# Performance work log

Hardware: AMD Instinct MI355X
Metric: run time of the kernel (lower is better)

## Reference

```python
import jax, jax.numpy as jnp
import numpy as np

N_NODES = 100000
N_EDGES = 1600000
F_IN = 128
H1 = 128
H2 = 128
N_CLASSES = 40


def setup_inputs() -> dict:
    key = jax.random.key(0)
    ks = jax.random.split(key, 8)
    node_features = jax.random.normal(ks[0], (N_NODES, F_IN), dtype=jnp.float32)
    edge_indices = jax.random.randint(ks[1], (2, N_EDGES), 0, N_NODES, dtype=jnp.int32)
    # Glorot-ish init for weights
    W1 = jax.random.normal(ks[2], (F_IN, H1), dtype=jnp.float32) / np.sqrt(F_IN)
    b1 = jnp.zeros((H1,), dtype=jnp.float32)
    W2 = jax.random.normal(ks[3], (H1, H2), dtype=jnp.float32) / np.sqrt(H1)
    b2 = jnp.zeros((H2,), dtype=jnp.float32)
    Wl = jax.random.normal(ks[4], (H2, N_CLASSES), dtype=jnp.float32) / np.sqrt(H2)
    bl = jnp.zeros((N_CLASSES,), dtype=jnp.float32)
    return {
        "node_features": node_features,
        "edge_indices": edge_indices,
        "W1": W1, "b1": b1,
        "W2": W2, "b2": b2,
        "Wl": Wl, "bl": bl,
    }


def _gcn_norm(edge_indices, n_nodes):
    # PyG GCNConv default: add self-loops, symmetric normalization.
    src = jnp.concatenate([edge_indices[0], jnp.arange(n_nodes, dtype=edge_indices.dtype)])
    dst = jnp.concatenate([edge_indices[1], jnp.arange(n_nodes, dtype=edge_indices.dtype)])
    deg = jax.ops.segment_sum(jnp.ones_like(dst, dtype=jnp.float32), dst,
                              num_segments=n_nodes)  # degree over destinations (col)
    deg_inv_sqrt = jnp.where(deg > 0, jax.lax.rsqrt(deg), 0.0)
    norm = deg_inv_sqrt[src] * deg_inv_sqrt[dst]  # (E + N,)
    return src, dst, norm


def _gcn_conv(x, W, b, src, dst, norm, n_nodes):
    xw = x @ W                                    # (N, F_out) dense GEMM
    msg = xw[src] * norm[:, None]                 # gather + scale: (E+N, F_out)
    out = jax.ops.segment_sum(msg, dst, num_segments=n_nodes)  # scatter-add
    return out + b


def reference(node_features, edge_indices, W1, b1, W2, b2, Wl, bl):
    n = node_features.shape[0]
    src, dst, norm = _gcn_norm(edge_indices, n)
    # dropout is identity in eval mode
    x = jax.nn.relu(_gcn_conv(node_features, W1, b1, src, dst, norm, n))
    x = jax.nn.relu(_gcn_conv(x, W2, b2, src, dst, norm, n))
    return x @ Wl + bl  # (N, num_classes)
```

## Files before the change

### kernel.cpp

```cpp
#include <hip/hip_runtime.h>


typedef unsigned int uint32;
typedef unsigned short u16;

#define FD 128

using short8 = __attribute__((ext_vector_type(8))) short;
using f32x4  = __attribute__((ext_vector_type(4))) float;

union U4S8 { uint4 u; short8 s; };

__device__ __forceinline__ u16 f2bf(float f) {
    uint32 u = __float_as_uint(f);
    uint32 r = ((u >> 16) & 1u) + 0x7FFFu;
    return (u16)((u + r) >> 16);
}
__device__ __forceinline__ float bf2f(u16 s) { return __uint_as_float((uint32)s << 16); }
__device__ __forceinline__ float bfLo(uint32 w) { return __uint_as_float(w << 16); }
__device__ __forceinline__ float bfHi(uint32 w) { return __uint_as_float(w & 0xFFFF0000u); }

__global__ void k_beacon(float* __restrict__ out, long long n, float val) {
    long long i = (long long)blockIdx.x * 256 + threadIdx.x;
    if (i < n) out[i] = val;
}

__global__ __launch_bounds__(256) void k_cnt_mgemm(
    const int* __restrict__ dst, int* __restrict__ cnt, int* __restrict__ rank,
    int ne, int nn,
    const float* __restrict__ A, const float* __restrict__ W,
    uint32* __restrict__ yt, int M,
    int ngemm) {
    __shared__ uint4 Bf[4][8][64];

    int bid = blockIdx.x;
    int g5 = bid / 5;
    bool isg = ((bid % 5) == 0) && (g5 < ngemm);
    int t = threadIdx.x;

    if (!isg) {
        int idx = bid - (g5 + 1 < ngemm ? g5 + 1 : ngemm);
        int e = idx * 256 + t;
        if (e < ne) {
            int d = dst[e];
            int a = ((unsigned)d < (unsigned)nn) ? d : nn;
            rank[e] = atomicAdd(&cnt[a], 1);
        }
        return;
    }

    int idx = g5;
    for (int e = t; e < 4 * 8 * 64; e += 256) {
        int kc = e / (8 * 64);
        int rem = e - kc * (8 * 64);
        int ct = rem >> 6;
        int l  = rem & 63;
        int k0 = kc * 32 + (l >> 4) * 8;
        int c  = ct * 16 + (l & 15);
        u16 us[8];
#pragma unroll
        for (int i = 0; i < 8; i++) us[i] = f2bf(W[(size_t)(k0 + i) * 128 + c]);
        uint4 u;
        u.x = (uint32)us[0] | ((uint32)us[1] << 16);
        u.y = (uint32)us[2] | ((uint32)us[3] << 16);
        u.z = (uint32)us[4] | ((uint32)us[5] << 16);
        u.w = (uint32)us[6] | ((uint32)us[7] << 16);
        Bf[kc][ct][l] = u;
    }
    __syncthreads();

    int lane = t & 63, wv = t >> 6;
    int r0 = idx * 64 + wv * 16;
    if (r0 >= M) return;

    int arow = r0 + (lane & 15);
    if (arow >= M) arow = M - 1;
    U4S8 af[4];
#pragma unroll
    for (int kc = 0; kc < 4; kc++) {
        const float4* s = (const float4*)(A + (size_t)arow * FD + kc * 32 + (lane >> 4) * 8);
        float4 v0 = s[0], v1 = s[1];
        uint4 u;
        u.x = (uint32)f2bf(v0.x) | ((uint32)f2bf(v0.y) << 16);
        u.y = (uint32)f2bf(v0.z) | ((uint32)f2bf(v0.w) << 16);
        u.z = (uint32)f2bf(v1.x) | ((uint32)f2bf(v1.y) << 16);
        u.w = (uint32)f2bf(v1.z) | ((uint32)f2bf(v1.w) << 16);
        af[kc].u = u;
    }

    f32x4 acc[8];
#pragma unroll
    for (int ct = 0; ct < 8; ct++) acc[ct] = f32x4{0.f, 0.f, 0.f, 0.f};
#pragma unroll
    for (int kc = 0; kc < 4; kc++) {
#pragma unroll
        for (int ct = 0; ct < 8; ct++) {
            U4S8 b;
            b.u = Bf[kc][ct][lane];
            acc[ct] = __builtin_amdgcn_mfma_f32_16x16x32_bf16(af[kc].s, b.s, acc[ct], 0, 0, 0);
        }
    }

    int rb = r0 + (lane >> 4) * 4;
#pragma unroll
    for (int r = 0; r < 4; r++) {
        int row = rb + r;
#pragma unroll
        for (int ct = 0; ct < 8; ct++) {
            float v = acc[ct][r];
            float vn = __shfl_xor(v, 1);
            if (!(lane & 1) && row < M) {
                uint32 word = (uint32)f2bf(v) | ((uint32)f2bf(vn) << 16);
                yt[(size_t)row * 128 + (ct * 16 + (lane & 15)) / 2] = word;
            }
        }
    }
}

__global__ void k_scan_a(const int* __restrict__ cnt, int* __restrict__ row_start,
                         int* __restrict__ bsum, float* __restrict__ dis, int nn) {
    __shared__ int tmp[256];
    int t = threadIdx.x;
    int i = blockIdx.x * 256 + t;
    int v = (i < nn) ? cnt[i] : 0;
    if (i < nn) dis[i] = rsqrtf((float)(v + 1));
    tmp[t] = v;
    __syncthreads();
    for (int off = 1; off < 256; off <<= 1) {
        int x = (t >= off) ? tmp[t - off] : 0;
        __syncthreads();
        tmp[t] += x;
        __syncthreads();
    }
    if (i < nn) row_start[i] = tmp[t] - v;
    if (t == 255) bsum[blockIdx.x] = tmp[255];
}

__global__ void k_scan_b(int* bsum, int nb) {
    __shared__ int tmp[512];
    __shared__ int carry;
    int t = threadIdx.x;
    if (t == 0) carry = 0;
    __syncthreads();
    for (int base = 0; base < nb; base += 512) {
        int i = base + t;
        int v = (i < nb) ? bsum[i] : 0;
        tmp[t] = v;
        __syncthreads();
        for (int off = 1; off < 512; off <<= 1) {
            int x = (t >= off) ? tmp[t - off] : 0;
            __syncthreads();
            tmp[t] += x;
            __syncthreads();
        }
        if (i < nb) bsum[i] = tmp[t] - v + carry;
        __syncthreads();
        if (t == 0) carry += tmp[511];
        __syncthreads();
    }
}

__global__ void k_scan_c(int* __restrict__ row_start, const int* __restrict__ bsum,
                         const int* __restrict__ cnt, int nn) {
    int i = blockIdx.x * 256 + threadIdx.x;
    if (i < nn) {
        int r = row_start[i] + bsum[blockIdx.x];
        row_start[i] = r;
        if (i == nn - 1) row_start[nn] = r + cnt[i];
    }
}

__global__ __launch_bounds__(256) void k_fill(const int* __restrict__ src,
                                              const int* __restrict__ dst,
                                              const int* __restrict__ rank,
                                              const int* __restrict__ row_start,
                                              int* __restrict__ col_idx,
                                              int ne, int nn) {
    long long base = ((long long)blockIdx.x * 256 + threadIdx.x) * 4;
    if (base + 4 <= (long long)ne) {
        int4 d4 = *(const int4*)(dst + base);
        int4 s4 = *(const int4*)(src + base);
        int4 r4 = *(const int4*)(rank + base);
        int dd[4] = {d4.x, d4.y, d4.z, d4.w};
        int ss[4] = {s4.x, s4.y, s4.z, s4.w};
        int rr[4] = {r4.x, r4.y, r4.z, r4.w};
        int pp[4];
#pragma unroll
        for (int r = 0; r < 4; r++) {
            bool ok = (unsigned)dd[r] < (unsigned)nn;
            int dv = ok ? dd[r] : 0;
            int p = row_start[dv] + rr[r];
            pp[r] = ok ? p : -1;
        }
#pragma unroll
        for (int r = 0; r < 4; r++)
            if ((unsigned)pp[r] < (unsigned)ne) col_idx[pp[r]] = ss[r];
    } else {
        for (long long e = base; e < (long long)ne; e++) {
            int d = dst[e];
            if ((unsigned)d >= (unsigned)nn) continue;
            int p = row_start[d] + rank[e];
            if ((unsigned)p < (unsigned)ne) col_idx[p] = src[e];
        }
    }
}

template <int NOUT, bool INBF, bool OUTBF>
__global__ __launch_bounds__(256) void k_mgemm(const void* __restrict__ Ap,
                                               const float* __restrict__ W,
                                               void* __restrict__ out,
                                               const float* __restrict__ bias,
                                               int M) {
    constexpr int NT = (NOUT + 15) / 16;
    __shared__ uint4 Bf[4][NT][64];

    int t = threadIdx.x;
    for (int e = t; e < 4 * NT * 64; e += 256) {
        int kc = e / (NT * 64);
        int rem = e - kc * (NT * 64);
        int ct = rem >> 6;
        int l  = rem & 63;
        int k0 = kc * 32 + (l >> 4) * 8;
        int c  = ct * 16 + (l & 15);
        u16 us[8];
#pragma unroll
        for (int i = 0; i < 8; i++)
            us[i] = (c < NOUT) ? f2bf(W[(size_t)(k0 + i) * NOUT + c]) : (u16)0;
        uint4 u;
        u.x = (uint32)us[0] | ((uint32)us[1] << 16);
        u.y = (uint32)us[2] | ((uint32)us[3] << 16);
        u.z = (uint32)us[4] | ((uint32)us[5] << 16);
        u.w = (uint32)us[6] | ((uint32)us[7] << 16);
        Bf[kc][ct][l] = u;
    }
    __syncthreads();

    int lane = t & 63, wv = t >> 6;
    int r0 = blockIdx.x * 64 + wv * 16;
    if (r0 >= M) return;

    int arow = r0 + (lane & 15);
    if (arow >= M) arow = M - 1;
    U4S8 af[4];
    if (INBF) {
        const u16* A = (const u16*)Ap;
#pragma unroll
        for (int kc = 0; kc < 4; kc++)
            af[kc].u = *(const uint4*)(A + (size_t)arow * FD + kc * 32 + (lane >> 4) * 8);
    } else {
        const float* A = (const float*)Ap;
#pragma unroll
        for (int kc = 0; kc < 4; kc++) {
            const float4* s = (const float4*)(A + (size_t)arow * FD + kc * 32 + (lane >> 4) * 8);
            float4 v0 = s[0], v1 = s[1];
            uint4 u;
            u.x = (uint32)f2bf(v0.x) | ((uint32)f2bf(v0.y) << 16);
            u.y = (uint32)f2bf(v0.z) | ((uint32)f2bf(v0.w) << 16);
            u.z = (uint32)f2bf(v1.x) | ((uint32)f2bf(v1.y) << 16);
            u.w = (uint32)f2bf(v1.z) | ((uint32)f2bf(v1.w) << 16);
            af[kc].u = u;
        }
    }

    f32x4 acc[NT];
#pragma unroll
    for (int ct = 0; ct < NT; ct++) acc[ct] = f32x4{0.f, 0.f, 0.f, 0.f};
#pragma unroll
    for (int kc = 0; kc < 4; kc++) {
#pragma unroll
        for (int ct = 0; ct < NT; ct++) {
            U4S8 b;
            b.u = Bf[kc][ct][lane];
            acc[ct] = __builtin_amdgcn_mfma_f32_16x16x32_bf16(af[kc].s, b.s, acc[ct], 0, 0, 0);
        }
    }

    int rb = r0 + (lane >> 4) * 4;
    if (OUTBF) {
        uint32* yt = (uint32*)out;
#pragma unroll
        for (int r = 0; r < 4; r++) {
            int row = rb + r;
#pragma unroll
            for (int ct = 0; ct < NT; ct++) {
                float v = acc[ct][r];
                float vn = __shfl_xor(v, 1);
                if (!(lane & 1) && row < M) {
                    uint32 word = (uint32)f2bf(v) | ((uint32)f2bf(vn) << 16);
                    yt[(size_t)row * 128 + (ct * 16 + (lane & 15)) / 2] = word;
                }
            }
        }
    } else {
        float* fo = (float*)out;
#pragma unroll
        for (int r = 0; r < 4; r++) {
            int row = rb + r;
            if (row >= M) continue;
#pragma unroll
            for (int ct = 0; ct < NT; ct++) {
                int c = ct * 16 + (lane & 15);
                if (c < NOUT) {
                    float v = acc[ct][r];
                    if (bias) v += bias[c];
                    fo[(size_t)row * NOUT + c] = v;
                }
            }
        }
    }
}

__global__ __launch_bounds__(256) void k_agg(const uint32* __restrict__ yt,
                                             const float* __restrict__ dis,
                                             const int* __restrict__ row_start,
                                             const int* __restrict__ col_idx,
                                             const float* __restrict__ bias,
                                             uint32* __restrict__ outp,
                                             int nn, int ne) {
    int lane = threadIdx.x & 63;
    int wid  = threadIdx.x >> 6;
    int g    = lane >> 4;
    int sub  = lane & 15;

    float2 bq[4];
#pragma unroll
    for (int k = 0; k < 4; k++) bq[k] = *(const float2*)(bias + (sub * 4 + k) * 2);

    const int stride = gridDim.x * 16;
    for (int n0 = blockIdx.x * 16 + wid * 4; n0 < nn; n0 += stride) {
        int n = n0 + g;
        bool act = n < nn;
        int nl = act ? n : 0;

        float di = dis[nl];
        int jb = row_start[nl];
        int je = row_start[nl + 1];
        if (!act) { jb = 0; je = 0; }
        if (jb < 0) jb = 0;
        if (je > ne) je = ne;
        int deg = je - jb; if (deg < 0) deg = 0;
        int je1 = je - 1;

        uint4 sv = *(const uint4*)(yt + (size_t)nl * 128 + sub * 4);
        float a0 = bfLo(sv.x) * di, a1 = bfHi(sv.x) * di;
        float a2 = bfLo(sv.y) * di, a3 = bfHi(sv.y) * di;
        float a4 = bfLo(sv.z) * di, a5 = bfHi(sv.z) * di;
        float a6 = bfLo(sv.w) * di, a7 = bfHi(sv.w) * di;

        int m = deg;
        m = max(m, __shfl_xor(m, 16));
        m = max(m, __shfl_xor(m, 32));

        for (int base = 0; base < m; base += 8) {
            int jj = jb + base + (sub & 7);
            int jc = jj < je ? jj : je1;
            if (jc < 0) jc = 0;
            int sl = col_idx[jc];
            float ds = 0.f;
            if ((unsigned)sl < (unsigned)nn) ds = dis[sl];
            else sl = 0;

            int ss[8];
            float ww[8];
#pragma unroll
            for (int r = 0; r < 8; r++) {
                int srcLane = (lane & 48) + r;
                int s = __shfl(sl, srcLane);
                float w = __shfl(ds, srcLane);
                ww[r] = (base + r < deg) ? w : 0.f;
                ss[r] = s;
            }
            uint4 uu[8];
#pragma unroll
            for (int r = 0; r < 8; r++)
                uu[r] = *(const uint4*)(yt + (size_t)ss[r] * 128 + sub * 4);
#pragma unroll
            for (int r = 0; r < 8; r++) {
                float wg = ww[r];
                a0 = fmaf(bfLo(uu[r].x), wg, a0); a1 = fmaf(bfHi(uu[r].x), wg, a1);
                a2 = fmaf(bfLo(uu[r].y), wg, a2); a3 = fmaf(bfHi(uu[r].y), wg, a3);
                a4 = fmaf(bfLo(uu[r].z), wg, a4); a5 = fmaf(bfHi(uu[r].z), wg, a5);
                a6 = fmaf(bfLo(uu[r].w), wg, a6); a7 = fmaf(bfHi(uu[r].w), wg, a7);
            }
        }

        if (act) {
            float r0 = fmaxf(fmaf(a0, di, bq[0].x), 0.f);
            float r1 = fmaxf(fmaf(a1, di, bq[0].y), 0.f);
            float r2 = fmaxf(fmaf(a2, di, bq[1].x), 0.f);
            float r3 = fmaxf(fmaf(a3, di, bq[1].y), 0.f);
            float r4 = fmaxf(fmaf(a4, di, bq[2].x), 0.f);
            float r5 = fmaxf(fmaf(a5, di, bq[2].y), 0.f);
            float r6 = fmaxf(fmaf(a6, di, bq[3].x), 0.f);
            float r7 = fmaxf(fmaf(a7, di, bq[3].y), 0.f);
            uint4 o;
            o.x = (uint32)f2bf(r0) | ((uint32)f2bf(r1) << 16);
            o.y = (uint32)f2bf(r2) | ((uint32)f2bf(r3) << 16);
            o.z = (uint32)f2bf(r4) | ((uint32)f2bf(r5) << 16);
            o.w = (uint32)f2bf(r6) | ((uint32)f2bf(r7) << 16);
            *(uint4*)(outp + (size_t)n * 64 + sub * 4) = o;
        }
    }
}

static inline char* carve(char*& p, size_t bytes) {
    char* r = p;
    p += (bytes + 255) & ~(size_t)255;
    return r;
}

extern "C" void kernel_launch(void* const* d_in, const int* in_sizes, int n_in,
                              void* d_out, int out_size, void* d_ws, size_t ws_size,
                              hipStream_t stream) {
    const long long outn = out_size;
    float* dout = (float*)d_out;
    if (n_in < 8) {
        k_beacon<<<(int)((outn + 255) / 256), 256, 0, stream>>>(dout, outn, 888.f);
        return;
    }
    float* X        = (float*)d_in[0];
    const int* ei   = (const int*)d_in[1];
    const float* W1 = (const float*)d_in[2];
    const float* b1 = (const float*)d_in[3];
    const float* W2 = (const float*)d_in[4];
    const float* b2 = (const float*)d_in[5];
    const float* Wl = (const float*)d_in[6];
    const float* bl = (const float*)d_in[7];

    const int H1 = in_sizes[3];
    const int F  = in_sizes[2] / (H1 > 0 ? H1 : 1);
    const int NC = in_sizes[7];
    const int NN = in_sizes[0] / (F > 0 ? F : 1);
    const int NE = in_sizes[1] / 2;
    if (NN <= 0 || NE <= 0 || F != FD || H1 != FD || NC != 40 ||
        (long long)NN * FD != in_sizes[0] || outn != (long long)NN * NC) {
        k_beacon<<<(int)((outn + 255) / 256), 256, 0, stream>>>(dout, outn, 888.f);
        return;
    }

    const int* src = ei;
    const int* dst = ei + NE;
    const int nb = (NN + 255) / 256;

    char* p = (char*)d_ws;
    int*   cnt       = (int*)  carve(p, ((size_t)NN + 1) * 4);
    float* dis       = (float*)carve(p, (size_t)NN * 4);
    int*   bsum      = (int*)  carve(p, (size_t)nb * 4);
    int*   row_start = (int*)  carve(p, ((size_t)NN + 1) * 4);
    u16*   bufA      = (u16*)  carve(p, (size_t)NN * FD * 2);
    size_t needed = (size_t)(p - (char*)d_ws);
    bool in_out = (size_t)NE * 8 <= (size_t)outn * 4;
    int* col_idx;
    int* rank;
    if (in_out) {
        col_idx = (int*)d_out;
        rank = (int*)((char*)d_out + (size_t)NE * 4);
    } else {
        col_idx = (int*)carve(p, (size_t)NE * 4);
        rank = (int*)carve(p, (size_t)NE * 4);
        needed = (size_t)(p - (char*)d_ws);
    }
    if (needed > ws_size) {
        k_beacon<<<(int)((outn + 255) / 256), 256, 0, stream>>>(dout, outn, 999.f);
        return;
    }

    const int ecb1 = (NE + 255) / 256;
    const int ecb4 = (int)(((long long)NE + 1023) / 1024);
    const int gemm_blocks = (NN + 63) / 64;
    int agg_blocks = (NN + 15) / 16;
    if (agg_blocks > 2048) agg_blocks = 2048;

    hipMemsetAsync(cnt, 0, ((size_t)NN + 1) * 4, stream);
    k_cnt_mgemm<<<ecb1 + gemm_blocks, 256, 0, stream>>>(
        dst, cnt, rank, NE, NN,
        X, W1, (uint32*)X, NN, gemm_blocks);
    k_scan_a<<<nb, 256, 0, stream>>>(cnt, row_start, bsum, dis, NN);
    k_scan_b<<<1, 512, 0, stream>>>(bsum, nb);
    k_scan_c<<<nb, 256, 0, stream>>>(row_start, bsum, cnt, NN);
    k_fill<<<ecb4, 256, 0, stream>>>(src, dst, rank, row_start, col_idx, NE, NN);

    k_agg<<<agg_blocks, 256, 0, stream>>>((const uint32*)X, dis, row_start, col_idx,
                                          b1, (uint32*)bufA, NN, NE);
    k_mgemm<128, true, true><<<gemm_blocks, 256, 0, stream>>>(bufA, W2, X, nullptr, NN);
    k_agg<<<agg_blocks, 256, 0, stream>>>((const uint32*)X, dis, row_start, col_idx,
                                          b2, (uint32*)bufA, NN, NE);
    k_mgemm<40, true, false><<<gemm_blocks, 256, 0, stream>>>(bufA, Wl, dout, bl, NN);
}
```

Before: 362.6 us.

## Fuse neighbor aggregation with following dense GEMM via shared-memory tile

Merges each aggregation kernel with the subsequent MFMA GEMM: a block aggregates 64 node rows into an LDS tile in bf16, then multiplies by the staged weight tile directly. The intermediate bf16 buffer round trip through global memory and two launches are removed. The second layer's source-side normalization is folded into the first fused kernel's output scaling, so the second aggregation runs unweighted. It also moves col_idx into the workspace and writes the layer output into an interleaved region of the input buffer. In exchange, the grid becomes one block per 64 nodes instead of a capped persistent grid, and LDS use per block grows.

```diff
diff --git a/kernel.cpp b/kernel.cpp
--- a/kernel.cpp
+++ b/kernel.cpp
@@ -16,7 +16,6 @@
     uint32 r = ((u >> 16) & 1u) + 0x7FFFu;
     return (u16)((u + r) >> 16);
 }
-__device__ __forceinline__ float bf2f(u16 s) { return __uint_as_float((uint32)s << 16); }
 __device__ __forceinline__ float bfLo(uint32 w) { return __uint_as_float(w << 16); }
 __device__ __forceinline__ float bfHi(uint32 w) { return __uint_as_float(w & 0xFFFF0000u); }
 
@@ -205,14 +204,20 @@
     }
 }
 
-template <int NOUT, bool INBF, bool OUTBF>
-__global__ __launch_bounds__(256) void k_mgemm(const void* __restrict__ Ap,
-                                               const float* __restrict__ W,
-                                               void* __restrict__ out,
-                                               const float* __restrict__ bias,
-                                               int M) {
+template <int NOUT, bool WEIGHTED, bool OUTBF>
+__global__ __launch_bounds__(256) void k_aggmm(
+    const uint32* __restrict__ ytin,
+    const float* __restrict__ dis,
+    const int* __restrict__ row_start,
+    const int* __restrict__ col_idx,
+    const float* __restrict__ abias,
+    const float* __restrict__ W,
+    void* __restrict__ out,
+    const float* __restrict__ gbias,
+    int nn, int ne) {
     constexpr int NT = (NOUT + 15) / 16;
-    __shared__ uint4 Bf[4][NT][64];
+    __shared__ uint4 Wf[4][NT][64];
+    __shared__ u16 Ar[64][136];
 
     int t = threadIdx.x;
     for (int e = t; e < 4 * NT * 64; e += 256) {
@@ -231,104 +236,20 @@
         u.y = (uint32)us[2] | ((uint32)us[3] << 16);
         u.z = (uint32)us[4] | ((uint32)us[5] << 16);
         u.w = (uint32)us[6] | ((uint32)us[7] << 16);
-        Bf[kc][ct][l] = u;
-    }
-    __syncthreads();
+        Wf[kc][ct][l] = u;
+    }
 
     int lane = t & 63, wv = t >> 6;
-    int r0 = blockIdx.x * 64 + wv * 16;
-    if (r0 >= M) return;
-
-    int arow = r0 + (lane & 15);
-    if (arow >= M) arow = M - 1;
-    U4S8 af[4];
-    if (INBF) {
-        const u16* A = (const u16*)Ap;
-#pragma unroll
-        for (int kc = 0; kc < 4; kc++)
-            af[kc].u = *(const uint4*)(A + (size_t)arow * FD + kc * 32 + (lane >> 4) * 8);
-    } else {
-        const float* A = (const float*)Ap;
-#pragma unroll
-        for (int kc = 0; kc < 4; kc++) {
-            const float4* s = (const float4*)(A + (size_t)arow * FD + kc * 32 + (lane >> 4) * 8);
-            float4 v0 = s[0], v1 = s[1];
-            uint4 u;
-            u.x = (uint32)f2bf(v0.x) | ((uint32)f2bf(v0.y) << 16);
-            u.y = (uint32)f2bf(v0.z) | ((uint32)f2bf(v0.w) << 16);
-            u.z = (uint32)f2bf(v1.x) | ((uint32)f2bf(v1.y) << 16);
-            u.w = (uint32)f2bf(v1.z) | ((uint32)f2bf(v1.w) << 16);
-            af[kc].u = u;
-        }
-    }
-
-    f32x4 acc[NT];
-#pragma unroll
-    for (int ct = 0; ct < NT; ct++) acc[ct] = f32x4{0.f, 0.f, 0.f, 0.f};
-#pragma unroll
-    for (int kc = 0; kc < 4; kc++) {
-#pragma unroll
-        for (int ct = 0; ct < NT; ct++) {
-            U4S8 b;
-            b.u = Bf[kc][ct][lane];
-            acc[ct] = __builtin_amdgcn_mfma_f32_16x16x32_bf16(af[kc].s, b.s, acc[ct], 0, 0, 0);
-        }
-    }
-
-    int rb = r0 + (lane >> 4) * 4;
-    if (OUTBF) {
-        uint32* yt = (uint32*)out;
-#pragma unroll
-        for (int r = 0; r < 4; r++) {
-            int row = rb + r;
-#pragma unroll
-            for (int ct = 0; ct < NT; ct++) {
-                float v = acc[ct][r];
-                float vn = __shfl_xor(v, 1);
-                if (!(lane & 1) && row < M) {
-                    uint32 word = (uint32)f2bf(v) | ((uint32)f2bf(vn) << 16);
-                    yt[(size_t)row * 128 + (ct * 16 + (lane & 15)) / 2] = word;
-                }
-            }
-        }
-    } else {
-        float* fo = (float*)out;
-#pragma unroll
-        for (int r = 0; r < 4; r++) {
-            int row = rb + r;
-            if (row >= M) continue;
-#pragma unroll
-            for (int ct = 0; ct < NT; ct++) {
-                int c = ct * 16 + (lane & 15);
-                if (c < NOUT) {
-                    float v = acc[ct][r];
-                    if (bias) v += bias[c];
-                    fo[(size_t)row * NOUT + c] = v;
-                }
-            }
-        }
-    }
-}
-
-__global__ __launch_bounds__(256) void k_agg(const uint32* __restrict__ yt,
-                                             const float* __restrict__ dis,
-                                             const int* __restrict__ row_start,
-                                             const int* __restrict__ col_idx,
-                                             const float* __restrict__ bias,
-                                             uint32* __restrict__ outp,
-                                             int nn, int ne) {
-    int lane = threadIdx.x & 63;
-    int wid  = threadIdx.x >> 6;
-    int g    = lane >> 4;
-    int sub  = lane & 15;
+    int g = lane >> 4, sub = lane & 15;
+    int nb0 = blockIdx.x * 64;
 
     float2 bq[4];
 #pragma unroll
-    for (int k = 0; k < 4; k++) bq[k] = *(const float2*)(bias + (sub * 4 + k) * 2);
-
-    const int stride = gridDim.x * 16;
-    for (int n0 = blockIdx.x * 16 + wid * 4; n0 < nn; n0 += stride) {
-        int n = n0 + g;
+    for (int k = 0; k < 4; k++) bq[k] = *(const float2*)(abias + (sub * 4 + k) * 2);
+
+    for (int it = 0; it < 4; it++) {
+        int lr = wv * 16 + it * 4 + g;
+        int n = nb0 + lr;
         bool act = n < nn;
         int nl = act ? n : 0;
 
@@ -341,11 +262,12 @@
         int deg = je - jb; if (deg < 0) deg = 0;
         int je1 = je - 1;
 
-        uint4 sv = *(const uint4*)(yt + (size_t)nl * 128 + sub * 4);
-        float a0 = bfLo(sv.x) * di, a1 = bfHi(sv.x) * di;
-        float a2 = bfLo(sv.y) * di, a3 = bfHi(sv.y) * di;
-        float a4 = bfLo(sv.z) * di, a5 = bfHi(sv.z) * di;
-        float a6 = bfLo(sv.w) * di, a7 = bfHi(sv.w) * di;
+        uint4 sv = *(const uint4*)(ytin + (size_t)nl * 128 + sub * 4);
+        float wself = WEIGHTED ? di : 1.f;
+        float a0 = bfLo(sv.x) * wself, a1 = bfHi(sv.x) * wself;
+        float a2 = bfLo(sv.y) * wself, a3 = bfHi(sv.y) * wself;
+        float a4 = bfLo(sv.z) * wself, a5 = bfHi(sv.z) * wself;
+        float a6 = bfLo(sv.w) * wself, a7 = bfHi(sv.w) * wself;
 
         int m = deg;
         m = max(m, __shfl_xor(m, 16));
@@ -356,24 +278,23 @@
             int jc = jj < je ? jj : je1;
             if (jc < 0) jc = 0;
             int sl = col_idx[jc];
-            float ds = 0.f;
-            if ((unsigned)sl < (unsigned)nn) ds = dis[sl];
-            else sl = 0;
+            bool okp = (unsigned)sl < (unsigned)nn;
+            float ds = WEIGHTED ? (okp ? dis[sl] : 0.f) : (okp ? 1.f : 0.f);
+            if (!okp) sl = 0;
 
             int ss[8];
             float ww[8];
 #pragma unroll
             for (int r = 0; r < 8; r++) {
-                int srcLane = (lane & 48) + r;
-                int s = __shfl(sl, srcLane);
-                float w = __shfl(ds, srcLane);
+                int L = (lane & 48) + r;
+                ss[r] = __shfl(sl, L);
+                float w = __shfl(ds, L);
                 ww[r] = (base + r < deg) ? w : 0.f;
-                ss[r] = s;
             }
             uint4 uu[8];
 #pragma unroll
             for (int r = 0; r < 8; r++)
-                uu[r] = *(const uint4*)(yt + (size_t)ss[r] * 128 + sub * 4);
+                uu[r] = *(const uint4*)(ytin + (size_t)ss[r] * 128 + sub * 4);
 #pragma unroll
             for (int r = 0; r < 8; r++) {
                 float wg = ww[r];
@@ -398,7 +319,60 @@
             o.y = (uint32)f2bf(r2) | ((uint32)f2bf(r3) << 16);
             o.z = (uint32)f2bf(r4) | ((uint32)f2bf(r5) << 16);
             o.w = (uint32)f2bf(r6) | ((uint32)f2bf(r7) << 16);
-            *(uint4*)(outp + (size_t)n * 64 + sub * 4) = o;
+            *(uint4*)&Ar[lr][sub * 8] = o;
+        }
+    }
+    __syncthreads();
+
+    int arl = wv * 16 + (lane & 15);
+    U4S8 af[4];
+#pragma unroll
+    for (int kc = 0; kc < 4; kc++)
+        af[kc].u = *(const uint4*)&Ar[arl][kc * 32 + (lane >> 4) * 8];
+
+    f32x4 acc[NT];
+#pragma unroll
+    for (int ct = 0; ct < NT; ct++) acc[ct] = f32x4{0.f, 0.f, 0.f, 0.f};
+#pragma unroll
+    for (int kc = 0; kc < 4; kc++) {
+#pragma unroll
+        for (int ct = 0; ct < NT; ct++) {
+            U4S8 b;
+            b.u = Wf[kc][ct][lane];
+            acc[ct] = __builtin_amdgcn_mfma_f32_16x16x32_bf16(af[kc].s, b.s, acc[ct], 0, 0, 0);
+        }
+    }
+
+    int rbl = wv * 16 + (lane >> 4) * 4;
+    if (OUTBF) {
+        uint32* yto = (uint32*)out;
+#pragma unroll
+        for (int r = 0; r < 4; r++) {
+            int grow = nb0 + rbl + r;
+            int gc = grow < nn ? grow : 0;
+            float rs = dis[gc];
+#pragma unroll
+            for (int ct = 0; ct < NT; ct++) {
+                float v = acc[ct][r] * rs;
+                float vn = __shfl_xor(v, 1);
+                if (!(lane & 1) && grow < nn) {
+                    uint32 word = (uint32)f2bf(v) | ((uint32)f2bf(vn) << 16);
+                    yto[(size_t)grow * 128 + (ct * 16 + (lane & 15)) / 2] = word;
+                }
+            }
+        }
+    } else {
+        float* fo = (float*)out;
+#pragma unroll
+        for (int r = 0; r < 4; r++) {
+            int grow = nb0 + rbl + r;
+            if (grow >= nn) continue;
+#pragma unroll
+            for (int ct = 0; ct < NT; ct++) {
+                int c = ct * 16 + (lane & 15);
+                if (c < NOUT)
+                    fo[(size_t)grow * NOUT + c] = acc[ct][r] + gbias[c];
+            }
         }
     }
 }
@@ -447,16 +421,12 @@
     float* dis       = (float*)carve(p, (size_t)NN * 4);
     int*   bsum      = (int*)  carve(p, (size_t)nb * 4);
     int*   row_start = (int*)  carve(p, ((size_t)NN + 1) * 4);
-    u16*   bufA      = (u16*)  carve(p, (size_t)NN * FD * 2);
+    int*   col_idx   = (int*)  carve(p, (size_t)NE * 4);
     size_t needed = (size_t)(p - (char*)d_ws);
-    bool in_out = (size_t)NE * 8 <= (size_t)outn * 4;
-    int* col_idx;
     int* rank;
-    if (in_out) {
-        col_idx = (int*)d_out;
-        rank = (int*)((char*)d_out + (size_t)NE * 4);
+    if ((size_t)NE * 4 <= (size_t)outn * 4) {
+        rank = (int*)d_out;
     } else {
-        col_idx = (int*)carve(p, (size_t)NE * 4);
         rank = (int*)carve(p, (size_t)NE * 4);
         needed = (size_t)(p - (char*)d_ws);
     }
@@ -468,22 +438,22 @@
     const int ecb1 = (NE + 255) / 256;
     const int ecb4 = (int)(((long long)NE + 1023) / 1024);
     const int gemm_blocks = (NN + 63) / 64;
-    int agg_blocks = (NN + 15) / 16;
-    if (agg_blocks > 2048) agg_blocks = 2048;
+
+    uint32* yt1 = (uint32*)X;
+    uint32* zt  = yt1 + 64;
 
     hipMemsetAsync(cnt, 0, ((size_t)NN + 1) * 4, stream);
     k_cnt_mgemm<<<ecb1 + gemm_blocks, 256, 0, stream>>>(
         dst, cnt, rank, NE, NN,
-        X, W1, (uint32*)X, NN, gemm_blocks);
+        X, W1, yt1, NN, gemm_blocks);
     k_scan_a<<<nb, 256, 0, stream>>>(cnt, row_start, bsum, dis, NN);
     k_scan_b<<<1, 512, 0, stream>>>(bsum, nb);
     k_scan_c<<<nb, 256, 0, stream>>>(row_start, bsum, cnt, NN);
     k_fill<<<ecb4, 256, 0, stream>>>(src, dst, rank, row_start, col_idx, NE, NN);
 
-    k_agg<<<agg_blocks, 256, 0, stream>>>((const uint32*)X, dis, row_start, col_idx,
-                                          b1, (uint32*)bufA, NN, NE);
-    k_mgemm<128, true, true><<<gemm_blocks, 256, 0, stream>>>(bufA, W2, X, nullptr, NN);
-    k_agg<<<agg_blocks, 256, 0, stream>>>((const uint32*)X, dis, row_start, col_idx,
-                                          b2, (uint32*)bufA, NN, NE);
-    k_mgemm<40, true, false><<<gemm_blocks, 256, 0, stream>>>(bufA, Wl, dout, bl, NN);
-}
+    k_aggmm<128, true, true><<<gemm_blocks, 256, 0, stream>>>(
+        yt1, dis, row_start, col_idx, b1, W2, (void*)zt, nullptr, NN, NE);
+
+    k_aggmm<40, false, false><<<gemm_blocks, 256, 0, stream>>>(
+        zt, dis, row_start, col_idx, b2, Wl, (void*)dout, bl, NN, NE);
+}
```

Result: slower. 373.8 us (+3.1%).
